# Kernel optimization log

Measured on AMD Instinct MI355X. Metric: run time of the kernel, lower is better.

The kernel has to match this reference:

```python
import jax, jax.numpy as jnp
import numpy as np

NPOINT = 1024
RADIUS = 0.15
NSAMPLE = 32
BN_EPS = 1e-5


def farthest_point_sample(xyz, npoint):
    # xyz: [B, N, 3] -> idx [B, npoint]
    B, N, _ = xyz.shape

    def step(carry, _):
        dmin, far = carry
        cent = jnp.take_along_axis(xyz, far[:, None, None], axis=1)  # [B,1,3]
        d = jnp.sum((xyz - cent) ** 2, axis=-1)                      # [B,N]
        dmin = jnp.minimum(dmin, d)
        nxt = jnp.argmax(dmin, axis=-1).astype(jnp.int32)
        return (dmin, nxt), far

    init = (jnp.full((B, N), 1e10, xyz.dtype), jnp.zeros((B,), jnp.int32))
    _, idx = jax.lax.scan(step, init, None, length=npoint)
    return idx.T  # [B, npoint]


def ball_query(radius, nsample, xyz, new_xyz):
    # xyz: [B,N,3], new_xyz: [B,S,3] -> idx [B,S,nsample]
    B, S, _ = new_xyz.shape
    N = xyz.shape[1]
    sqr = jnp.sum((new_xyz[:, :, None, :] - xyz[:, None, :, :]) ** 2, axis=-1)  # [B,S,N]
    ar = jnp.broadcast_to(jnp.arange(N, dtype=jnp.int32), (B, S, N))
    gidx = jnp.where(sqr > radius * radius, N, ar)
    gidx = jnp.sort(gidx, axis=-1)[:, :, :nsample]
    first = gidx[:, :, :1]
    return jnp.where(gidx == N, first, gidx)


def setup_inputs() -> dict:
    key = jax.random.key(0)
    ks = jax.random.split(key, 8)
    B, N, Cin, Cmlp, Cout = 8, 4096, 64, 128, 256
    xyz = jax.random.uniform(ks[0], (B, N, 3), dtype=jnp.float32)
    t = jax.random.normal(ks[1], (B, 128), dtype=jnp.float32)
    points = jax.random.normal(ks[2], (B, N, Cin), dtype=jnp.float32)
    W1 = jax.random.normal(ks[3], (Cin, Cmlp), dtype=jnp.float32) / np.sqrt(Cin)
    b1 = jnp.zeros((Cmlp,), jnp.float32)
    Wc = jax.random.normal(ks[4], (Cmlp, Cout), dtype=jnp.float32) / np.sqrt(Cmlp)
    bc = jnp.zeros((Cout,), jnp.float32)
    gamma = jnp.ones((Cout,), jnp.float32)
    beta = jnp.zeros((Cout,), jnp.float32)
    return {"xyz": xyz, "t": t, "points": points, "W1": W1, "b1": b1,
            "Wc": Wc, "bc": bc, "gamma": gamma, "beta": beta}


def reference(xyz, t, points, W1, b1, Wc, bc, gamma, beta):
    # t (time embedding) is unused in the visible (truncated) forward body.
    B, N, _ = xyz.shape
    # 1) farthest point sampling -> centers
    fps_idx = farthest_point_sample(xyz, NPOINT)                     # [B,S]
    new_xyz = jnp.take_along_axis(xyz, fps_idx[:, :, None], axis=1)  # [B,S,3]
    # 2) radius ball-query grouping
    gidx = ball_query(RADIUS, NSAMPLE, xyz, new_xyz)                 # [B,S,ns]
    # 3) pointwise MLP on features, then group (gather)
    feats = points @ W1 + b1                                          # [B,N,Cmlp]
    grouped = jax.vmap(lambda f, i: f[i])(feats, gidx)                # [B,S,ns,Cmlp]
    # 4) GroupConv: 1x1 conv + BatchNorm(train stats) + ReLU
    h = jnp.einsum('bsnc,co->bsno', grouped, Wc) + bc                 # [B,S,ns,Cout]
    mean = jnp.mean(h, axis=(0, 1, 2))
    var = jnp.var(h, axis=(0, 1, 2))
    h = jax.nn.relu((h - mean) / jnp.sqrt(var + BN_EPS) * gamma + beta)
    # 5) max-pool over neighborhood
    new_points = jnp.max(h, axis=2)                                   # [B,S,Cout]
    return new_points
```

## Files before the change

### kernel.cpp

```cpp
#include <hip/hip_runtime.h>
#include <stdint.h>

#define BN 8
#define NPT 4096
#define NS 1024
#define KS 32
#define CIN 64
#define CMID 128
#define COUT 256
#define NGRP (BN*NS)
#define NBINS 512

typedef short bf16x8 __attribute__((ext_vector_type(8)));
typedef float f32x4 __attribute__((ext_vector_type(4)));
typedef unsigned long long u64;

__device__ __forceinline__ float bf2f(unsigned short u){
  union { unsigned int i; float f; } v; v.i = ((unsigned int)u) << 16; return v.f;
}
__device__ __forceinline__ unsigned short f2bf(float f){
  union { float f; unsigned int i; } v; v.f = f;
  unsigned int r = (v.i + 0x7fffu + ((v.i >> 16) & 1u)) >> 16;
  return (unsigned short)r;
}
__device__ __forceinline__ uint32_t pack2(float a, float b){
  return (uint32_t)f2bf(a) | ((uint32_t)f2bf(b) << 16);
}
__device__ __forceinline__ float ldf(const void* p, size_t i, bool isbf){
  return isbf ? bf2f(((const unsigned short*)p)[i]) : ((const float*)p)[i];
}
__device__ __forceinline__ bool detect_bf(const void* gamma){
  return ((const unsigned int*)gamma)[0] == 0x3F803F80u;
}
template<int CTRL>
__device__ __forceinline__ u64 dpp_u64(u64 x){
  int lo = (int)(unsigned int)(x & 0xFFFFFFFFull);
  int hi = (int)(unsigned int)(x >> 32);
  int nlo = __builtin_amdgcn_update_dpp(0, lo, CTRL, 0xF, 0xF, true);
  int nhi = __builtin_amdgcn_update_dpp(0, hi, CTRL, 0xF, 0xF, true);
  return ((u64)(unsigned int)nhi << 32) | (unsigned int)nlo;
}
__device__ __forceinline__ u64 u64max(u64 a, u64 b){ return a > b ? a : b; }
__device__ __forceinline__ u64 wave_max_u64(u64 k){
  k = u64max(k, dpp_u64<0x121>(k));
  k = u64max(k, dpp_u64<0x122>(k));
  k = u64max(k, dpp_u64<0x124>(k));
  k = u64max(k, dpp_u64<0x128>(k));
  k = u64max(k, dpp_u64<0x142>(k));
  k = u64max(k, dpp_u64<0x143>(k));
  return k;
}
__device__ __forceinline__ u64 readlane63_u64(u64 k){
  unsigned lo = (unsigned)__builtin_amdgcn_readlane((int)(unsigned)(k & 0xFFFFFFFFull), 63);
  unsigned hi = (unsigned)__builtin_amdgcn_readlane((int)(unsigned)(k >> 32), 63);
  return ((u64)hi << 32) | lo;
}
__device__ __forceinline__ void bbox6(float x, float y, float z,
                                      float&xl,float&xh,float&yl,float&yh,float&zl,float&zh){
  xl=x; xh=x; yl=y; yh=y; zl=z; zh=z;
  #pragma unroll
  for (int off=1; off<64; off<<=1){
    xl=fminf(xl,__shfl_xor(xl,off,64)); xh=fmaxf(xh,__shfl_xor(xh,off,64));
    yl=fminf(yl,__shfl_xor(yl,off,64)); yh=fmaxf(yh,__shfl_xor(yh,off,64));
    zl=fminf(zl,__shfl_xor(zl,off,64)); zh=fmaxf(zh,__shfl_xor(zh,off,64));
  }
}

__device__ __forceinline__ unsigned mcode(float x, float y, float z){
  int ix = (int)(x*16.f); ix = ix<0?0:(ix>15?15:ix);
  int iy = (int)(y*16.f); iy = iy<0?0:(iy>15?15:iy);
  int iz = (int)(z*8.f);  iz = iz<0?0:(iz>7?7:iz);
  return ((unsigned)(iy&1))      | ((unsigned)(ix&1)<<1) | ((unsigned)(iz&1)<<2)
       | ((unsigned)(iy&2)<<2)   | ((unsigned)(ix&2)<<3) | ((unsigned)(iz&2)<<4)
       | ((unsigned)(iy&4)<<4)   | ((unsigned)(ix&4)<<5) | ((unsigned)(iz&4)<<6)
       | ((unsigned)(iy&8)<<6)   | ((unsigned)(ix&8)<<7);
}

__global__ __launch_bounds__(512, 3)
void k_front(const void* __restrict__ xyz,
             const void* __restrict__ points,
             const void* __restrict__ W1,
             const void* __restrict__ Wc,
             const void* __restrict__ gamma,
             float* __restrict__ newxyz,
             unsigned short* __restrict__ featsb,
             unsigned short* __restrict__ wct,
             float* __restrict__ ps, float* __restrict__ pq, int bigws)
{
  int tid = threadIdx.x;
  int bid = blockIdx.x;
  bool isbf = detect_bf(gamma);
  __shared__ __align__(16) char smem[65536];
  __shared__ unsigned tsum[512];
  __shared__ u64 wk[2][8];

  if (bid < 8){
    float* ssx = (float*)smem;
    float* ssy = ssx + NPT;
    float* ssz = ssy + NPT;
    unsigned short* snl = (unsigned short*)(ssz + NPT);
    unsigned* hist = (unsigned*)(smem + 57344);
    size_t xb = (size_t)bid*NPT*3;
    int base = tid*8;
    for (int i=tid; i<2048; i+=512) hist[i]=0;
    __syncthreads();
    unsigned codes[8];
    #pragma unroll
    for (int k=0;k<8;k++){
      size_t p = xb + (size_t)(base+k)*3;
      unsigned c = mcode(ldf(xyz,p,isbf), ldf(xyz,p+1,isbf), ldf(xyz,p+2,isbf));
      codes[k]=c;
      atomicAdd(&hist[c],1u);
    }
    __syncthreads();
    unsigned l0=hist[tid*4],l1=hist[tid*4+1],l2=hist[tid*4+2],l3=hist[tid*4+3];
    unsigned s = l0+l1+l2+l3;
    tsum[tid]=s; __syncthreads();
    for (int off=1; off<512; off<<=1){
      unsigned v = (tid>=off)? tsum[tid-off]:0u; __syncthreads();
      tsum[tid]+=v; __syncthreads();
    }
    unsigned ex0 = tsum[tid]-s;
    hist[tid*4]=ex0; hist[tid*4+1]=ex0+l0; hist[tid*4+2]=ex0+l0+l1; hist[tid*4+3]=ex0+l0+l1+l2;
    __syncthreads();
    #pragma unroll
    for (int k=0;k<8;k++){
      size_t p = xb + (size_t)(base+k)*3;
      float x=ldf(xyz,p,isbf), y=ldf(xyz,p+1,isbf), z=ldf(xyz,p+2,isbf);
      unsigned pos = atomicAdd(&hist[codes[k]],1u);
      ssx[pos]=x; ssy[pos]=y; ssz[pos]=z; snl[pos]=(unsigned short)(4095-(base+k));
    }
    __syncthreads();
    int lane = tid & 63, wv = tid >> 6;
    float qx0,qx1,qx2,qx3,qx4,qx5,qx6,qx7;
    float qy0,qy1,qy2,qy3,qy4,qy5,qy6,qy7;
    float qz0,qz1,qz2,qz3,qz4,qz5,qz6,qz7;
    float dd0,dd1,dd2,dd3,dd4,dd5,dd6,dd7;
    unsigned lk0,lk1,lk2,lk3,lk4,lk5,lk6,lk7;
#define LOADS(k) { int p = (wv<<9) + ((k)<<6) + lane; \
  qx##k=ssx[p]; qy##k=ssy[p]; qz##k=ssz[p]; dd##k=1e10f; \
  lk##k = ((unsigned)snl[p]<<12) | (unsigned)p; }
    LOADS(0) LOADS(1) LOADS(2) LOADS(3) LOADS(4) LOADS(5) LOADS(6) LOADS(7)
#undef LOADS
    float qbxl=0.f,qbxh=0.f,qbyl=0.f,qbyh=0.f,qbzl=0.f,qbzh=0.f;
    int lq = lane & 7;
#define CB(k) { float xl,xh,yl,yh,zl,zh; bbox6(qx##k,qy##k,qz##k,xl,xh,yl,yh,zl,zh); \
  if (lq==(k)){ qbxl=xl; qbxh=xh; qbyl=yl; qbyh=yh; qbzl=zl; qbzh=zh; } }
    CB(0) CB(1) CB(2) CB(3) CB(4) CB(5) CB(6) CB(7)
#undef CB
    float cx=ldf(xyz,xb,isbf), cy=ldf(xyz,xb+1,isbf), cz=ldf(xyz,xb+2,isbf);
    if (tid==0){ float* o = newxyz + (size_t)bid*NS*3; o[0]=cx; o[1]=cy; o[2]=cz; }
    u64 ckey = ((u64)__float_as_uint(1e10f) << 32);
    for (int it=1; it<NS; ++it){
      int par = it & 1;
      float exd = fmaxf(fmaxf(__fsub_rn(qbxl,cx), __fsub_rn(cx,qbxh)), 0.f);
      float eyd = fmaxf(fmaxf(__fsub_rn(qbyl,cy), __fsub_rn(cy,qbyh)), 0.f);
      float ezd = fmaxf(fmaxf(__fsub_rn(qbzl,cz), __fsub_rn(cz,qbzh)), 0.f);
      float lb2 = exd*exd + eyd*eyd + ezd*ezd;
      float wtmax = __uint_as_float((unsigned)(ckey >> 32));
      unsigned amask = (unsigned)__ballot(lb2*0.999f < wtmax) & 0xFFu;
      if (amask){
#define FPS_STEP(k) if (amask & (1u<<(k))){ \
  float dx=__fsub_rn(qx##k,cx), dy=__fsub_rn(qy##k,cy), dz=__fsub_rn(qz##k,cz); \
  float d=__fadd_rn(__fadd_rn(__fmul_rn(dx,dx),__fmul_rn(dy,dy)),__fmul_rn(dz,dz)); \
  dd##k=fminf(dd##k,d); }
        FPS_STEP(0) FPS_STEP(1) FPS_STEP(2) FPS_STEP(3)
        FPS_STEP(4) FPS_STEP(5) FPS_STEP(6) FPS_STEP(7)
#undef FPS_STEP
#define KEYK(k) ( ((u64)__float_as_uint(dd##k) << 32) | lk##k )
        u64 t0=u64max(KEYK(0),KEYK(1)), t2=u64max(KEYK(2),KEYK(3));
        u64 t4=u64max(KEYK(4),KEYK(5)), t6=u64max(KEYK(6),KEYK(7));
#undef KEYK
        t0=u64max(t0,t2); t4=u64max(t4,t6);
        u64 key = u64max(t0,t4);
        ckey = readlane63_u64(wave_max_u64(key));
      }
      if (lane == 0) wk[par][wv] = ckey;
      __syncthreads();
      const u64* w8 = wk[par];
      u64 k0 = u64max(u64max(u64max(w8[0],w8[1]), u64max(w8[2],w8[3])),
                      u64max(u64max(w8[4],w8[5]), u64max(w8[6],w8[7])));
      unsigned spos = (unsigned)(k0 & 0xFFFu);
      cx = ssx[spos]; cy = ssy[spos]; cz = ssz[spos];
      if (tid==0){ float* o = newxyz + ((size_t)bid*NS + it)*3; o[0]=cx; o[1]=cy; o[2]=cz; }
    }
  } else if (bid == 8){
    for (int i=tid; i<CMID*COUT; i+=512){
      int k = i >> 8, n = i & 255;
      unsigned short w = isbf ? ((const unsigned short*)Wc)[i] : f2bf(((const float*)Wc)[i]);
      wct[(size_t)n*CMID + k] = w;
    }
    if (!bigws){
      for (int i=tid; i<COUT*NBINS; i+=512){ ps[i]=0.f; pq[i]=0.f; }
    }
  } else {
    float* w1s = (float*)smem;
    float* pts = (float*)(smem + 32768);
    int rb = bid - 9;
    int r0g = rb*64;
    for (int i=tid; i<CIN*CMID; i+=512) w1s[i] = ldf(W1, i, isbf);
    for (int i=tid; i<64*CIN; i+=512)   pts[i] = ldf(points, (size_t)r0g*CIN + i, isbf);
    __syncthreads();
    int o0 = (tid & 15) * 8, r0 = (tid >> 4) * 2;
    float acc0[8]={0,0,0,0,0,0,0,0}, acc1[8]={0,0,0,0,0,0,0,0};
    for (int c=0;c<CIN;c++){
      float a0 = pts[r0*CIN + c], a1 = pts[(r0+1)*CIN + c];
      const float* wr = &w1s[c*CMID + o0];
      #pragma unroll
      for (int j=0;j<8;j++){ acc0[j] = fmaf(a0, wr[j], acc0[j]); acc1[j] = fmaf(a1, wr[j], acc1[j]); }
    }
    unsigned short* f0 = featsb + ((size_t)(r0g + r0))*CMID + o0;
    uint4 u;
    u.x=pack2(acc0[0],acc0[1]); u.y=pack2(acc0[2],acc0[3]); u.z=pack2(acc0[4],acc0[5]); u.w=pack2(acc0[6],acc0[7]);
    *(uint4*)f0 = u;
    u.x=pack2(acc1[0],acc1[1]); u.y=pack2(acc1[2],acc1[3]); u.z=pack2(acc1[4],acc1[5]); u.w=pack2(acc1[6],acc1[7]);
    *(uint4*)(f0 + CMID) = u;
  }
}

__global__ __launch_bounds__(256)
void k_groupq(const void* __restrict__ xyz,
              const float* __restrict__ newxyz,
              const unsigned short* __restrict__ featsb,
              const unsigned short* __restrict__ wct,
              const void* __restrict__ gamma,
              float* __restrict__ ps, float* __restrict__ pq,
              float* __restrict__ hM, int bigws)
{
  int tid = threadIdx.x;
  int bs0 = blockIdx.x * 2;
  int b = bs0 >> 10;
  bool isbf = detect_bf(gamma);
  __shared__ __align__(16) char smem[49152];
  __shared__ int gi[2][KS];
  int lane = tid & 63, wv = tid >> 6;

  float* sp = (float*)smem;
  size_t xb = (size_t)b*NPT*3;
  for (int i=tid; i<NPT*3; i+=256) sp[i] = ldf(xyz, xb + i, isbf);
  __syncthreads();

  if (wv < 2){
    int cid = bs0 + wv;
    const float* cc = newxyz + (size_t)cid*3;
    float cx=cc[0], cy=cc[1], cz=cc[2];
    const float rr = (float)(0.15*0.15);
    int cnt = 0;
    for (int ch=0; ch<64; ++ch){
      int p = ch*64 + lane;
      float dx=__fsub_rn(sp[p*3],cx), dy=__fsub_rn(sp[p*3+1],cy), dz=__fsub_rn(sp[p*3+2],cz);
      float d=__fadd_rn(__fadd_rn(__fmul_rn(dx,dx),__fmul_rn(dy,dy)),__fmul_rn(dz,dz));
      bool in = !(d > rr);
      u64 mk = __ballot(in);
      int pos = cnt + __popcll(mk & ((1ull<<lane) - 1ull));
      if (in && pos < KS) gi[wv][pos] = p;
      cnt += __popcll(mk);
      if (cnt >= KS) break;
    }
    int total = cnt < KS ? cnt : KS;
    if (lane < KS){
      int v = (lane < total) ? gi[wv][lane] : gi[wv][0];
      gi[wv][lane] = v;
    }
  }
  __syncthreads();

  typedef unsigned short grow_t[32][136];
  grow_t* g = (grow_t*)smem;
  {
    int r = tid >> 3, sg = tid & 7;
    size_t fb = (size_t)b*NPT;
    int gi0 = gi[0][r], gi1 = gi[1][r];
    const unsigned short* s0 = featsb + (fb + gi0)*CMID + sg*16;
    const unsigned short* s1 = featsb + (fb + gi1)*CMID + sg*16;
    uint4 a0 = *(const uint4*)s0, a1 = *(const uint4*)(s0 + 8);
    uint4 b0 = *(const uint4*)s1, b1 = *(const uint4*)(s1 + 8);
    *(uint4*)(&g[0][r][sg*16])     = a0;
    *(uint4*)(&g[0][r][sg*16 + 8]) = a1;
    *(uint4*)(&g[1][r][sg*16])     = b0;
    *(uint4*)(&g[1][r][sg*16 + 8]) = b1;
  }
  __syncthreads();

  int m = lane & 15, quad = lane >> 4;
  f32x4 acc[2][2][4];
  #pragma unroll
  for (int gg=0; gg<2; gg++)
    #pragma unroll
    for (int a=0;a<2;a++)
      #pragma unroll
      for (int b2=0;b2<4;b2++) acc[gg][a][b2] = (f32x4){0.f,0.f,0.f,0.f};
  int n0 = wv * 64;
  #pragma unroll
  for (int k0=0; k0<CMID; k0+=32){
    bf16x8 a00 = *(const bf16x8*)(&g[0][m][k0 + quad*8]);
    bf16x8 a01 = *(const bf16x8*)(&g[0][16 + m][k0 + quad*8]);
    bf16x8 a10 = *(const bf16x8*)(&g[1][m][k0 + quad*8]);
    bf16x8 a11 = *(const bf16x8*)(&g[1][16 + m][k0 + quad*8]);
    #pragma unroll
    for (int nt=0; nt<4; nt++){
      int n = n0 + nt*16 + m;
      bf16x8 bb = *(const bf16x8*)(wct + (size_t)n*CMID + k0 + quad*8);
      acc[0][0][nt] = __builtin_amdgcn_mfma_f32_16x16x32_bf16(a00, bb, acc[0][0][nt], 0, 0, 0);
      acc[0][1][nt] = __builtin_amdgcn_mfma_f32_16x16x32_bf16(a01, bb, acc[0][1][nt], 0, 0, 0);
      acc[1][0][nt] = __builtin_amdgcn_mfma_f32_16x16x32_bf16(a10, bb, acc[1][0][nt], 0, 0, 0);
      acc[1][1][nt] = __builtin_amdgcn_mfma_f32_16x16x32_bf16(a11, bb, acc[1][1][nt], 0, 0, 0);
    }
  }
  #pragma unroll
  for (int gg=0; gg<2; gg++){
    int bs = bs0 + gg;
    #pragma unroll
    for (int nt=0; nt<4; nt++){
      float s=0.f, q=0.f, hx=-3.402823466e38f;
      #pragma unroll
      for (int mt=0; mt<2; mt++)
        #pragma unroll
        for (int rg=0; rg<4; rg++){ float h = acc[gg][mt][nt][rg]; s += h; q += h*h; hx = fmaxf(hx,h); }
      s += __shfl_xor(s,16,64); q += __shfl_xor(q,16,64); hx = fmaxf(hx, __shfl_xor(hx,16,64));
      s += __shfl_xor(s,32,64); q += __shfl_xor(q,32,64); hx = fmaxf(hx, __shfl_xor(hx,32,64));
      if (quad == 0){
        int o = n0 + nt*16 + m;
        if (bigws){
          ps[(size_t)o*NGRP + bs] = s;
          pq[(size_t)o*NGRP + bs] = q;
        } else {
          atomicAdd(&ps[(size_t)o*NBINS + (bs & (NBINS-1))], s);
          atomicAdd(&pq[(size_t)o*NBINS + (bs & (NBINS-1))], q);
        }
        hM[(size_t)bs*COUT + o] = hx;
      }
    }
  }
}

__global__ __launch_bounds__(256)
void k_bn(const float* __restrict__ ps, const float* __restrict__ pq,
          const float* __restrict__ hM,
          const void* __restrict__ gamma, const void* __restrict__ beta,
          void* __restrict__ out, int nbins)
{
  int tid = threadIdx.x, o = blockIdx.x;
  bool isbf = detect_bf(gamma);
  float s=0.f, q=0.f;
  for (int i=tid; i<nbins; i+=256){ s += ps[(size_t)o*nbins + i]; q += pq[(size_t)o*nbins + i]; }
  #pragma unroll
  for (int off=1; off<64; off<<=1){ s += __shfl_xor(s,off,64); q += __shfl_xor(q,off,64); }
  __shared__ float ls[4], lq[4], sa, sc;
  int lane = tid & 63, wv = tid >> 6;
  if (lane == 0){ ls[wv]=s; lq[wv]=q; }
  __syncthreads();
  if (tid == 0){
    float S = ls[0]+ls[1]+ls[2]+ls[3], Q = lq[0]+lq[1]+lq[2]+lq[3];
    const float invM = 1.0f/262144.0f;
    float mean = S*invM;
    float var  = fmaxf(Q*invM - mean*mean, 0.f);
    float inv  = 1.0f/sqrtf(var + 1e-5f);
    float a = ldf(gamma,o,isbf)*inv;
    float c = ldf(beta,o,isbf) - mean*a;
    sa=a; sc=c;
  }
  __syncthreads();
  float a = sa, c = sc;
  for (int bs=tid; bs<NGRP; bs+=256){
    size_t oi = (size_t)bs*COUT + o;
    float v = fmaxf(hM[oi]*a + c, 0.f);
    if (isbf) ((unsigned short*)out)[oi] = f2bf(v);
    else      ((float*)out)[oi] = v;
  }
}

extern "C" void kernel_launch(void* const* d_in, const int* in_sizes, int n_in,
                              void* d_out, int out_size, void* d_ws, size_t ws_size,
                              hipStream_t stream)
{
  const void* xyz    = d_in[0];
  const void* points = d_in[2];
  const void* W1     = d_in[3];
  const void* Wc     = d_in[5];
  const void* gamma  = d_in[7];
  const void* beta   = d_in[8];

  char* ws = (char*)d_ws;
  unsigned short* featsb = (unsigned short*)(ws + 0);
  unsigned short* wct    = (unsigned short*)(ws + 8388608);
  float* newxyz          = (float*)(ws + 8454144);
  bool bigws = ws_size >= (size_t)34768896;
  float *ps, *pq, *hM;
  if (bigws){
    ps = (float*)(ws + 9601024);
    pq = (float*)(ws + 17989632);
    hM = (float*)(ws + 26378240);
  } else {
    hM = (float*)(ws + 9601024);
    ps = (float*)(ws + 17989632);
    pq = (float*)(ws + 18513920);
  }

  hipLaunchKernelGGL(k_front,  dim3(521), dim3(512), 0, stream,
                     xyz, points, W1, Wc, gamma, newxyz, featsb, wct, ps, pq, (int)bigws);
  hipLaunchKernelGGL(k_groupq, dim3(4096), dim3(256), 0, stream,
                     xyz, newxyz, featsb, wct, gamma, ps, pq, hM, (int)bigws);
  hipLaunchKernelGGL(k_bn,     dim3(256),  dim3(256), 0, stream,
                     ps, pq, hM, gamma, beta, d_out, bigws ? NGRP : NBINS);
}
```

Baseline: 907.0 us.

## Fuse front and grouping kernels into a flag-synchronized producer/consumer megakernel

Merges the FPS/feature-GEMM front kernel and the ball-query/grouped-GEMM kernel into one launch. Consumer blocks spin on per-batch FPS progress counters and a GEMM completion counter, so grouping work can start while FPS is still producing centers. A fallback kernel reruns any consumer whose wait timed out, and a memset clears the flags each call. This adds spin-wait traffic, extra launches and wider 512-thread blocks where only 256 threads do consumer work, and it depends on the producer blocks being resident before the consumers.

```diff
diff --git a/kernel.cpp b/kernel.cpp
--- a/kernel.cpp
+++ b/kernel.cpp
@@ -10,6 +10,8 @@
 #define COUT 256
 #define NGRP (BN*NS)
 #define NBINS 512
+#define NCONS 4096
+#define GEMMN 513
 
 typedef short bf16x8 __attribute__((ext_vector_type(8)));
 typedef float f32x4 __attribute__((ext_vector_type(4)));
@@ -65,7 +67,6 @@
     zl=fminf(zl,__shfl_xor(zl,off,64)); zh=fmaxf(zh,__shfl_xor(zh,off,64));
   }
 }
-
 __device__ __forceinline__ unsigned mcode(float x, float y, float z){
   int ix = (int)(x*16.f); ix = ix<0?0:(ix>15?15:ix);
   int iy = (int)(y*16.f); iy = iy<0?0:(iy>15?15:iy);
@@ -76,16 +77,132 @@
        | ((unsigned)(iy&8)<<6)   | ((unsigned)(ix&8)<<7);
 }
 
-__global__ __launch_bounds__(512, 3)
-void k_front(const void* __restrict__ xyz,
-             const void* __restrict__ points,
-             const void* __restrict__ W1,
-             const void* __restrict__ Wc,
-             const void* __restrict__ gamma,
-             float* __restrict__ newxyz,
-             unsigned short* __restrict__ featsb,
-             unsigned short* __restrict__ wct,
-             float* __restrict__ ps, float* __restrict__ pq, int bigws)
+__device__ __forceinline__ void consumer_work(
+    char* smem, int (*gi)[KS], int bs0,
+    const void* __restrict__ xyz, const float* __restrict__ newxyz,
+    const unsigned short* __restrict__ featsb, const unsigned short* __restrict__ wct,
+    bool isbf, float* __restrict__ ps, float* __restrict__ pq,
+    float* __restrict__ hM, int bigws)
+{
+  int tid = threadIdx.x;
+  int nthr = blockDim.x;
+  int b = bs0 >> 10;
+  int lane = tid & 63, wv = tid >> 6;
+
+  float* sp = (float*)smem;
+  size_t xb = (size_t)b*NPT*3;
+  for (int i=tid; i<NPT*3; i+=nthr) sp[i] = ldf(xyz, xb + i, isbf);
+  __syncthreads();
+
+  if (wv < 2){
+    int cid = bs0 + wv;
+    const float* cc = newxyz + (size_t)cid*3;
+    float cx=cc[0], cy=cc[1], cz=cc[2];
+    const float rr = (float)(0.15*0.15);
+    int cnt = 0;
+    for (int ch=0; ch<64; ++ch){
+      int p = ch*64 + lane;
+      float dx=__fsub_rn(sp[p*3],cx), dy=__fsub_rn(sp[p*3+1],cy), dz=__fsub_rn(sp[p*3+2],cz);
+      float d=__fadd_rn(__fadd_rn(__fmul_rn(dx,dx),__fmul_rn(dy,dy)),__fmul_rn(dz,dz));
+      bool in = !(d > rr);
+      u64 mk = __ballot(in);
+      int pos = cnt + __popcll(mk & ((1ull<<lane) - 1ull));
+      if (in && pos < KS) gi[wv][pos] = p;
+      cnt += __popcll(mk);
+      if (cnt >= KS) break;
+    }
+    int total = cnt < KS ? cnt : KS;
+    if (lane < KS){
+      int v = (lane < total) ? gi[wv][lane] : gi[wv][0];
+      gi[wv][lane] = v;
+    }
+  }
+  __syncthreads();
+
+  typedef unsigned short grow_t[32][136];
+  grow_t* g = (grow_t*)smem;
+  if (tid < 256){
+    int r = tid >> 3, sg = tid & 7;
+    size_t fb = (size_t)b*NPT;
+    int gi0 = gi[0][r], gi1 = gi[1][r];
+    const unsigned short* s0p = featsb + (fb + gi0)*CMID + sg*16;
+    const unsigned short* s1p = featsb + (fb + gi1)*CMID + sg*16;
+    uint4 a0 = *(const uint4*)s0p, a1 = *(const uint4*)(s0p + 8);
+    uint4 b0 = *(const uint4*)s1p, b1 = *(const uint4*)(s1p + 8);
+    *(uint4*)(&g[0][r][sg*16])     = a0;
+    *(uint4*)(&g[0][r][sg*16 + 8]) = a1;
+    *(uint4*)(&g[1][r][sg*16])     = b0;
+    *(uint4*)(&g[1][r][sg*16 + 8]) = b1;
+  }
+  __syncthreads();
+
+  if (tid < 256){
+    int m = lane & 15, quad = lane >> 4;
+    f32x4 acc[2][2][4];
+    #pragma unroll
+    for (int gg=0; gg<2; gg++)
+      #pragma unroll
+      for (int a=0;a<2;a++)
+        #pragma unroll
+        for (int b2=0;b2<4;b2++) acc[gg][a][b2] = (f32x4){0.f,0.f,0.f,0.f};
+    int n0 = wv * 64;
+    #pragma unroll
+    for (int k0=0; k0<CMID; k0+=32){
+      bf16x8 a00 = *(const bf16x8*)(&g[0][m][k0 + quad*8]);
+      bf16x8 a01 = *(const bf16x8*)(&g[0][16 + m][k0 + quad*8]);
+      bf16x8 a10 = *(const bf16x8*)(&g[1][m][k0 + quad*8]);
+      bf16x8 a11 = *(const bf16x8*)(&g[1][16 + m][k0 + quad*8]);
+      #pragma unroll
+      for (int nt=0; nt<4; nt++){
+        int n = n0 + nt*16 + m;
+        bf16x8 bb = *(const bf16x8*)(wct + (size_t)n*CMID + k0 + quad*8);
+        acc[0][0][nt] = __builtin_amdgcn_mfma_f32_16x16x32_bf16(a00, bb, acc[0][0][nt], 0, 0, 0);
+        acc[0][1][nt] = __builtin_amdgcn_mfma_f32_16x16x32_bf16(a01, bb, acc[0][1][nt], 0, 0, 0);
+        acc[1][0][nt] = __builtin_amdgcn_mfma_f32_16x16x32_bf16(a10, bb, acc[1][0][nt], 0, 0, 0);
+        acc[1][1][nt] = __builtin_amdgcn_mfma_f32_16x16x32_bf16(a11, bb, acc[1][1][nt], 0, 0, 0);
+      }
+    }
+    #pragma unroll
+    for (int gg=0; gg<2; gg++){
+      int bs = bs0 + gg;
+      #pragma unroll
+      for (int nt=0; nt<4; nt++){
+        float s=0.f, q=0.f, hx=-3.402823466e38f;
+        #pragma unroll
+        for (int mt=0; mt<2; mt++)
+          #pragma unroll
+          for (int rg=0; rg<4; rg++){ float h = acc[gg][mt][nt][rg]; s += h; q += h*h; hx = fmaxf(hx,h); }
+        s += __shfl_xor(s,16,64); q += __shfl_xor(q,16,64); hx = fmaxf(hx, __shfl_xor(hx,16,64));
+        s += __shfl_xor(s,32,64); q += __shfl_xor(q,32,64); hx = fmaxf(hx, __shfl_xor(hx,32,64));
+        if (quad == 0){
+          int o = n0 + nt*16 + m;
+          if (bigws){
+            ps[(size_t)o*NGRP + bs] = s;
+            pq[(size_t)o*NGRP + bs] = q;
+          } else {
+            atomicAdd(&ps[(size_t)o*NBINS + (bs & (NBINS-1))], s);
+            atomicAdd(&pq[(size_t)o*NBINS + (bs & (NBINS-1))], q);
+          }
+          hM[(size_t)bs*COUT + o] = hx;
+        }
+      }
+    }
+  }
+}
+
+__global__ __launch_bounds__(512, 2)
+void k_mega(const void* __restrict__ xyz,
+            const void* __restrict__ points,
+            const void* __restrict__ W1,
+            const void* __restrict__ Wc,
+            const void* __restrict__ gamma,
+            float* __restrict__ newxyz,
+            unsigned short* __restrict__ featsb,
+            unsigned short* __restrict__ wct,
+            float* __restrict__ ps, float* __restrict__ pq,
+            float* __restrict__ hM,
+            int* __restrict__ progress, unsigned* __restrict__ gemmc,
+            int* __restrict__ done, int bigws)
 {
   int tid = threadIdx.x;
   int bid = blockIdx.x;
@@ -93,6 +210,8 @@
   __shared__ __align__(16) char smem[65536];
   __shared__ unsigned tsum[512];
   __shared__ u64 wk[2][8];
+  __shared__ int gi[2][KS];
+  __shared__ int sh_ok;
 
   if (bid < 8){
     float* ssx = (float*)smem;
@@ -182,7 +301,13 @@
                       u64max(u64max(w8[4],w8[5]), u64max(w8[6],w8[7])));
       unsigned spos = (unsigned)(k0 & 0xFFFu);
       cx = ssx[spos]; cy = ssy[spos]; cz = ssz[spos];
-      if (tid==0){ float* o = newxyz + ((size_t)bid*NS + it)*3; o[0]=cx; o[1]=cy; o[2]=cz; }
+      if (tid==0){
+        float* o = newxyz + ((size_t)bid*NS + it)*3; o[0]=cx; o[1]=cy; o[2]=cz;
+        if (((it & 15) == 15) || it == NS-1){
+          __threadfence();
+          __hip_atomic_store(&progress[bid], it+1, __ATOMIC_RELAXED, __HIP_MEMORY_SCOPE_AGENT);
+        }
+      }
     }
   } else if (bid == 8){
     for (int i=tid; i<CMID*COUT; i+=512){
@@ -193,7 +318,10 @@
     if (!bigws){
       for (int i=tid; i<COUT*NBINS; i+=512){ ps[i]=0.f; pq[i]=0.f; }
     }
-  } else {
+    __syncthreads();
+    if (tid==0){ __threadfence();
+      __hip_atomic_fetch_add(gemmc, 1u, __ATOMIC_RELAXED, __HIP_MEMORY_SCOPE_AGENT); }
+  } else if (bid < 9+512){
     float* w1s = (float*)smem;
     float* pts = (float*)(smem + 32768);
     int rb = bid - 9;
@@ -215,123 +343,45 @@
     *(uint4*)f0 = u;
     u.x=pack2(acc1[0],acc1[1]); u.y=pack2(acc1[2],acc1[3]); u.z=pack2(acc1[4],acc1[5]); u.w=pack2(acc1[6],acc1[7]);
     *(uint4*)(f0 + CMID) = u;
-  }
-}
-
-__global__ __launch_bounds__(256)
-void k_groupq(const void* __restrict__ xyz,
-              const float* __restrict__ newxyz,
-              const unsigned short* __restrict__ featsb,
-              const unsigned short* __restrict__ wct,
-              const void* __restrict__ gamma,
-              float* __restrict__ ps, float* __restrict__ pq,
-              float* __restrict__ hM, int bigws)
+    __syncthreads();
+    if (tid==0){ __threadfence();
+      __hip_atomic_fetch_add(gemmc, 1u, __ATOMIC_RELAXED, __HIP_MEMORY_SCOPE_AGENT); }
+  } else {
+    int ci = bid - (9+512);
+    int bs0 = ci*2;
+    int b = bs0 >> 10;
+    int s0 = bs0 & 1023;
+    if (tid==0){
+      int ok=1, iters=0;
+      for(;;){
+        unsigned gq = __hip_atomic_load(gemmc, __ATOMIC_RELAXED, __HIP_MEMORY_SCOPE_AGENT);
+        int pr = __hip_atomic_load(&progress[b], __ATOMIC_RELAXED, __HIP_MEMORY_SCOPE_AGENT);
+        if (gq >= (unsigned)GEMMN && pr >= s0+2) break;
+        __builtin_amdgcn_s_sleep(32);
+        if (++iters > 4000){ ok=0; break; }
+      }
+      if (ok) __threadfence();
+      sh_ok = ok;
+    }
+    __syncthreads();
+    if (!sh_ok) return;
+    consumer_work(smem, gi, bs0, xyz, newxyz, featsb, wct, isbf, ps, pq, hM, bigws);
+    if (tid==0) done[ci] = 1;
+  }
+}
+
+__global__ __launch_bounds__(512)
+void k_fix(const void* __restrict__ xyz, const float* __restrict__ newxyz,
+           const unsigned short* __restrict__ featsb, const unsigned short* __restrict__ wct,
+           const void* __restrict__ gamma,
+           float* __restrict__ ps, float* __restrict__ pq, float* __restrict__ hM,
+           const int* __restrict__ done, int bigws)
 {
-  int tid = threadIdx.x;
-  int bs0 = blockIdx.x * 2;
-  int b = bs0 >> 10;
-  bool isbf = detect_bf(gamma);
   __shared__ __align__(16) char smem[49152];
   __shared__ int gi[2][KS];
-  int lane = tid & 63, wv = tid >> 6;
-
-  float* sp = (float*)smem;
-  size_t xb = (size_t)b*NPT*3;
-  for (int i=tid; i<NPT*3; i+=256) sp[i] = ldf(xyz, xb + i, isbf);
-  __syncthreads();
-
-  if (wv < 2){
-    int cid = bs0 + wv;
-    const float* cc = newxyz + (size_t)cid*3;
-    float cx=cc[0], cy=cc[1], cz=cc[2];
-    const float rr = (float)(0.15*0.15);
-    int cnt = 0;
-    for (int ch=0; ch<64; ++ch){
-      int p = ch*64 + lane;
-      float dx=__fsub_rn(sp[p*3],cx), dy=__fsub_rn(sp[p*3+1],cy), dz=__fsub_rn(sp[p*3+2],cz);
-      float d=__fadd_rn(__fadd_rn(__fmul_rn(dx,dx),__fmul_rn(dy,dy)),__fmul_rn(dz,dz));
-      bool in = !(d > rr);
-      u64 mk = __ballot(in);
-      int pos = cnt + __popcll(mk & ((1ull<<lane) - 1ull));
-      if (in && pos < KS) gi[wv][pos] = p;
-      cnt += __popcll(mk);
-      if (cnt >= KS) break;
-    }
-    int total = cnt < KS ? cnt : KS;
-    if (lane < KS){
-      int v = (lane < total) ? gi[wv][lane] : gi[wv][0];
-      gi[wv][lane] = v;
-    }
-  }
-  __syncthreads();
-
-  typedef unsigned short grow_t[32][136];
-  grow_t* g = (grow_t*)smem;
-  {
-    int r = tid >> 3, sg = tid & 7;
-    size_t fb = (size_t)b*NPT;
-    int gi0 = gi[0][r], gi1 = gi[1][r];
-    const unsigned short* s0 = featsb + (fb + gi0)*CMID + sg*16;
-    const unsigned short* s1 = featsb + (fb + gi1)*CMID + sg*16;
-    uint4 a0 = *(const uint4*)s0, a1 = *(const uint4*)(s0 + 8);
-    uint4 b0 = *(const uint4*)s1, b1 = *(const uint4*)(s1 + 8);
-    *(uint4*)(&g[0][r][sg*16])     = a0;
-    *(uint4*)(&g[0][r][sg*16 + 8]) = a1;
-    *(uint4*)(&g[1][r][sg*16])     = b0;
-    *(uint4*)(&g[1][r][sg*16 + 8]) = b1;
-  }
-  __syncthreads();
-
-  int m = lane & 15, quad = lane >> 4;
-  f32x4 acc[2][2][4];
-  #pragma unroll
-  for (int gg=0; gg<2; gg++)
-    #pragma unroll
-    for (int a=0;a<2;a++)
-      #pragma unroll
-      for (int b2=0;b2<4;b2++) acc[gg][a][b2] = (f32x4){0.f,0.f,0.f,0.f};
-  int n0 = wv * 64;
-  #pragma unroll
-  for (int k0=0; k0<CMID; k0+=32){
-    bf16x8 a00 = *(const bf16x8*)(&g[0][m][k0 + quad*8]);
-    bf16x8 a01 = *(const bf16x8*)(&g[0][16 + m][k0 + quad*8]);
-    bf16x8 a10 = *(const bf16x8*)(&g[1][m][k0 + quad*8]);
-    bf16x8 a11 = *(const bf16x8*)(&g[1][16 + m][k0 + quad*8]);
-    #pragma unroll
-    for (int nt=0; nt<4; nt++){
-      int n = n0 + nt*16 + m;
-      bf16x8 bb = *(const bf16x8*)(wct + (size_t)n*CMID + k0 + quad*8);
-      acc[0][0][nt] = __builtin_amdgcn_mfma_f32_16x16x32_bf16(a00, bb, acc[0][0][nt], 0, 0, 0);
-      acc[0][1][nt] = __builtin_amdgcn_mfma_f32_16x16x32_bf16(a01, bb, acc[0][1][nt], 0, 0, 0);
-      acc[1][0][nt] = __builtin_amdgcn_mfma_f32_16x16x32_bf16(a10, bb, acc[1][0][nt], 0, 0, 0);
-      acc[1][1][nt] = __builtin_amdgcn_mfma_f32_16x16x32_bf16(a11, bb, acc[1][1][nt], 0, 0, 0);
-    }
-  }
-  #pragma unroll
-  for (int gg=0; gg<2; gg++){
-    int bs = bs0 + gg;
-    #pragma unroll
-    for (int nt=0; nt<4; nt++){
-      float s=0.f, q=0.f, hx=-3.402823466e38f;
-      #pragma unroll
-      for (int mt=0; mt<2; mt++)
-        #pragma unroll
-        for (int rg=0; rg<4; rg++){ float h = acc[gg][mt][nt][rg]; s += h; q += h*h; hx = fmaxf(hx,h); }
-      s += __shfl_xor(s,16,64); q += __shfl_xor(q,16,64); hx = fmaxf(hx, __shfl_xor(hx,16,64));
-      s += __shfl_xor(s,32,64); q += __shfl_xor(q,32,64); hx = fmaxf(hx, __shfl_xor(hx,32,64));
-      if (quad == 0){
-        int o = n0 + nt*16 + m;
-        if (bigws){
-          ps[(size_t)o*NGRP + bs] = s;
-          pq[(size_t)o*NGRP + bs] = q;
-        } else {
-          atomicAdd(&ps[(size_t)o*NBINS + (bs & (NBINS-1))], s);
-          atomicAdd(&pq[(size_t)o*NBINS + (bs & (NBINS-1))], q);
-        }
-        hM[(size_t)bs*COUT + o] = hx;
-      }
-    }
-  }
+  int ci = blockIdx.x;
+  if (done[ci]) return;
+  consumer_work(smem, gi, ci*2, xyz, newxyz, featsb, wct, detect_bf(gamma), ps, pq, hM, bigws);
 }
 
 __global__ __launch_bounds__(256)
@@ -385,6 +435,9 @@
   unsigned short* featsb = (unsigned short*)(ws + 0);
   unsigned short* wct    = (unsigned short*)(ws + 8388608);
   float* newxyz          = (float*)(ws + 8454144);
+  int*      progress = (int*)(ws + 8552448);
+  unsigned* gemmc    = (unsigned*)(ws + 8552480);
+  int*      done     = (int*)(ws + 8552512);
   bool bigws = ws_size >= (size_t)34768896;
   float *ps, *pq, *hM;
   if (bigws){
@@ -397,10 +450,13 @@
     pq = (float*)(ws + 18513920);
   }
 
-  hipLaunchKernelGGL(k_front,  dim3(521), dim3(512), 0, stream,
-                     xyz, points, W1, Wc, gamma, newxyz, featsb, wct, ps, pq, (int)bigws);
-  hipLaunchKernelGGL(k_groupq, dim3(4096), dim3(256), 0, stream,
-                     xyz, newxyz, featsb, wct, gamma, ps, pq, hM, (int)bigws);
-  hipLaunchKernelGGL(k_bn,     dim3(256),  dim3(256), 0, stream,
+  (void)hipMemsetAsync(ws + 8552448, 0, 64 + NCONS*sizeof(int), stream);
+
+  hipLaunchKernelGGL(k_mega, dim3(9 + 512 + NCONS), dim3(512), 0, stream,
+                     xyz, points, W1, Wc, gamma, newxyz, featsb, wct,
+                     ps, pq, hM, progress, gemmc, done, (int)bigws);
+  hipLaunchKernelGGL(k_fix,  dim3(NCONS), dim3(512), 0, stream,
+                     xyz, newxyz, featsb, wct, gamma, ps, pq, hM, done, (int)bigws);
+  hipLaunchKernelGGL(k_bn,   dim3(256),  dim3(256), 0, stream,
                      ps, pq, hM, gamma, beta, d_out, bigws ? NGRP : NBINS);
 }
```

New measurement: 998.6 us. 1.1x slower.
